# Kernel tuning notes

Hardware: AMD Instinct MI355X
Metric: run time of the kernel (lower is better)

## Reference

```python
import jax, jax.numpy as jnp
import numpy as np

STRIDE = 1  # module init arg


def setup_inputs() -> dict:
    key = jax.random.key(0)
    k1, k2 = jax.random.split(key)
    x = jax.random.normal(k1, (16, 32, 256, 256), dtype=jnp.float32)
    kernel = jax.random.normal(k2, (32, 5, 5), dtype=jnp.float32) * 0.1
    return {"input": x, "kernel": kernel}


def _maxmin_conv(x, kernel, stride=STRIDE):
    # Max-min semifield convolution:
    #   out[b,oc,i,j] = max_{c,dy,dx} min(x_pad[b,c,i*s+dy,j*s+dx], k[oc,dy,dx])
    # Since min(., k) is monotone in x, the max over in-channels commutes:
    #   max_{c} min(x_c, k) == min(max_c x_c, k)
    # so we reduce channels once up front (same math, far less memory).
    K = kernel.shape[-1]
    p = K - 1
    top = p // 2
    bot = p - top  # calculate_padding(): left=top=floor(p/2), right=bottom=p-top
    xmax = jnp.max(x, axis=1)  # [B, H, W]
    xp = jnp.pad(xmax, ((0, 0), (top, bot), (top, bot)), constant_values=-np.inf)
    B, Hp, Wp = xp.shape
    Ho = (Hp - K) // stride + 1
    Wo = (Wp - K) // stride + 1
    OC = kernel.shape[0]
    acc = jnp.full((B, OC, Ho, Wo), -np.inf, dtype=x.dtype)
    for dy in range(K):  # fixed small K*K loop over kernel taps
        for dx in range(K):
            patch = xp[:, dy:dy + stride * Ho:stride, dx:dx + stride * Wo:stride]  # [B,Ho,Wo]
            cand = jnp.minimum(patch[:, None, :, :], kernel[None, :, dy, dx, None, None])
            acc = jnp.maximum(acc, cand)
    return acc


def reference(input, kernel):
    return _maxmin_conv(input, kernel)
```

## Files before the change

### kernel.cpp

```cpp
#include <hip/hip_runtime.h>
#include <math.h>


#define BATCH 16
#define CH    32
#define OCH   32
#define HH    256
#define WW    256
#define HWSZ  (HH * WW)
#define TW    32
#define TH    16
#define LH    20
#define LW    42
#define KP    28
#define NWG   (BATCH * (HH / TH) * (WW / TW))

typedef float floatx4 __attribute__((ext_vector_type(4)));

__device__ __forceinline__ float vmax3(float a, float b, float c) {
    float d;
    asm("v_max3_f32 %0, %1, %2, %3" : "=v"(d) : "v"(a), "v"(b), "v"(c));
    return d;
}

__global__ __launch_bounds__(256, 2) void fused_maxmin_kernel(const float* __restrict__ x,
                                                              const float* __restrict__ kk,
                                                              float* __restrict__ out) {
    __shared__ float xmt[LH][LW];
    __shared__ float lk[OCH * KP];
    int tid = threadIdx.x;
    int bid = blockIdx.x;
    int swz = (bid & 7) * (NWG >> 3) + (bid >> 3);
    int b   = swz >> 7;
    int t2  = swz & 127;
    int ty  = t2 >> 3;
    int tx  = t2 & 7;

    const float NI = -INFINITY;

    for (int i = tid; i < OCH * 25; i += 256)
        lk[(i / 25) * KP + (i % 25)] = kk[i];

    if (tid < 200) {
        int pr = tid / 10;
        int pc = tid % 10;
        int c4 = tx * 8 - 1 + pc;
        int rw = ty * TH - 2 + pr;
        bool valid = (c4 >= 0) && (c4 < WW / 4) && (rw >= 0) && (rw < HH);
        int c4c = c4 < 0 ? 0 : (c4 > WW / 4 - 1 ? WW / 4 - 1 : c4);
        int rwc = rw < 0 ? 0 : (rw > HH - 1 ? HH - 1 : rw);
        const float4* src = (const float4*)x + (size_t)b * CH * (HWSZ / 4)
                          + (size_t)rwc * (WW / 4) + c4c;
        float4 m = src[0];
#pragma unroll
        for (int c = 1; c < CH; ++c) {
            float4 v = src[(size_t)c * (HWSZ / 4)];
            m.x = fmaxf(m.x, v.x);
            m.y = fmaxf(m.y, v.y);
            m.z = fmaxf(m.z, v.z);
            m.w = fmaxf(m.w, v.w);
        }
        if (!valid) { m.x = NI; m.y = NI; m.z = NI; m.w = NI; }
        *(float2*)&xmt[pr][4 * pc]     = make_float2(m.x, m.y);
        *(float2*)&xmt[pr][4 * pc + 2] = make_float2(m.z, m.w);
    }
    __syncthreads();

    int xg = tid & 7;
    int rg = (tid >> 3) & 7;
    int wv = __builtin_amdgcn_readfirstlane(tid >> 6);

    float w[6][8];
#pragma unroll
    for (int r = 0; r < 6; ++r) {
        const float* rp = &xmt[2 * rg + r][4 * xg + 2];
#pragma unroll
        for (int s = 0; s < 4; ++s)
            *(float2*)&w[r][2 * s] = *(const float2*)(rp + 2 * s);
    }

    size_t obase = (size_t)(b * OCH + wv * 8) * HWSZ
                 + (size_t)(ty * TH + 2 * rg) * WW + tx * TW + 4 * xg;

    for (int o = 0; o < 8; ++o) {
        const float* kv = &lk[(wv * 8 + o) * KP];
        float4 q0 = *(const float4*)(kv + 0);
        float4 q1 = *(const float4*)(kv + 4);
        float4 q2 = *(const float4*)(kv + 8);
        float4 q3 = *(const float4*)(kv + 12);
        float4 q4 = *(const float4*)(kv + 16);
        float4 q5 = *(const float4*)(kv + 20);
        float  k24 = kv[24];
        float kr[25] = { q0.x,q0.y,q0.z,q0.w, q1.x,q1.y,q1.z,q1.w,
                         q2.x,q2.y,q2.z,q2.w, q3.x,q3.y,q3.z,q3.w,
                         q4.x,q4.y,q4.z,q4.w, q5.x,q5.y,q5.z,q5.w, k24 };

        float* op = out + obase + (size_t)o * HWSZ;
#pragma unroll
        for (int r = 0; r < 2; ++r) {
            float a[4];
#pragma unroll
            for (int j = 0; j < 4; ++j) {
                float m[25];
#pragma unroll
                for (int dy = 0; dy < 5; ++dy)
#pragma unroll
                    for (int dx = 0; dx < 5; ++dx)
                        m[dy * 5 + dx] = fminf(w[r + dy][j + dx], kr[dy * 5 + dx]);
                float t0 = vmax3(m[0],  m[1],  m[2]);
                float t1 = vmax3(m[3],  m[4],  m[5]);
                float t2 = vmax3(m[6],  m[7],  m[8]);
                float t3 = vmax3(m[9],  m[10], m[11]);
                float t4 = vmax3(m[12], m[13], m[14]);
                float t5 = vmax3(m[15], m[16], m[17]);
                float t6 = vmax3(m[18], m[19], m[20]);
                float t7 = vmax3(m[21], m[22], m[23]);
                float u0 = vmax3(t0, t1, t2);
                float u1 = vmax3(t3, t4, t5);
                float u2 = vmax3(t6, t7, m[24]);
                a[j] = vmax3(u0, u1, u2);
            }
            floatx4 ov = { a[0], a[1], a[2], a[3] };
            __builtin_nontemporal_store(ov, (floatx4*)(op + (size_t)r * WW));
        }
    }
}

extern "C" void kernel_launch(void* const* d_in, const int* in_sizes, int n_in,
                              void* d_out, int out_size, void* d_ws, size_t ws_size,
                              hipStream_t stream) {
    const float* x  = (const float*)d_in[0];
    const float* kk = (const float*)d_in[1];
    float* out      = (float*)d_out;
    fused_maxmin_kernel<<<NWG, 256, 0, stream>>>(x, kk, out);
}
```

Before: 55.27 us.

## Warp-specialize into producer waves and consumer waves with double-buffered LDS tiles

Each workgroup now covers four vertical 16-row tiles and runs 640 threads. Two waves perform the channel-max reduction into a double-buffered shared tile, and eight waves compute the 32 output channels, four each. The intent is to overlap the global-load-heavy reduction with the compute and store phase of the previous tile and to cut the grid to 512 workgroups. The risks are lower occupancy from 640-thread blocks, and the producer waves may become the bottleneck because only 128 threads issue all input loads.

```diff
diff --git a/kernel.cpp b/kernel.cpp
--- a/kernel.cpp
+++ b/kernel.cpp
@@ -8,12 +8,11 @@
 #define HH    256
 #define WW    256
 #define HWSZ  (HH * WW)
-#define TW    32
-#define TH    16
 #define LH    20
 #define LW    42
 #define KP    28
-#define NWG   (BATCH * (HH / TH) * (WW / TW))
+#define NT    4
+#define NWG   512
 
 typedef float floatx4 __attribute__((ext_vector_type(4)));
 
@@ -23,105 +22,150 @@
     return d;
 }
 
-__global__ __launch_bounds__(256, 2) void fused_maxmin_kernel(const float* __restrict__ x,
+__device__ __forceinline__ void lgkm_barrier() {
+    asm volatile("s_waitcnt lgkmcnt(0)" ::: "memory");
+    __builtin_amdgcn_s_barrier();
+}
+
+__global__ __launch_bounds__(640, 5) void fused_maxmin_kernel(const float* __restrict__ x,
                                                               const float* __restrict__ kk,
                                                               float* __restrict__ out) {
-    __shared__ float xmt[LH][LW];
+    __shared__ float xmt[2][LH][LW];
     __shared__ float lk[OCH * KP];
+
     int tid = threadIdx.x;
     int bid = blockIdx.x;
     int swz = (bid & 7) * (NWG >> 3) + (bid >> 3);
-    int b   = swz >> 7;
-    int t2  = swz & 127;
-    int ty  = t2 >> 3;
-    int tx  = t2 & 7;
+    int b   = swz >> 5;
+    int s   = swz & 31;
+    int ys  = s >> 3;
+    int xs  = s & 7;
+    int row0 = ys * 64;
 
     const float NI = -INFINITY;
 
-    for (int i = tid; i < OCH * 25; i += 256)
+    for (int i = tid; i < OCH * 25; i += 640)
         lk[(i / 25) * KP + (i % 25)] = kk[i];
 
-    if (tid < 200) {
-        int pr = tid / 10;
-        int pc = tid % 10;
-        int c4 = tx * 8 - 1 + pc;
-        int rw = ty * TH - 2 + pr;
-        bool valid = (c4 >= 0) && (c4 < WW / 4) && (rw >= 0) && (rw < HH);
-        int c4c = c4 < 0 ? 0 : (c4 > WW / 4 - 1 ? WW / 4 - 1 : c4);
-        int rwc = rw < 0 ? 0 : (rw > HH - 1 ? HH - 1 : rw);
-        const float4* src = (const float4*)x + (size_t)b * CH * (HWSZ / 4)
-                          + (size_t)rwc * (WW / 4) + c4c;
-        float4 m = src[0];
+    const float4* xb4 = (const float4*)x + (size_t)b * CH * (HWSZ / 4);
+    int wave = tid >> 6;
+
+    if (wave < 2) {
+        int pr1 = tid / 10,        pc1 = tid % 10;
+        int g2  = tid + 128;
+        bool has2 = tid < 72;
+        int pr2 = g2 / 10,         pc2 = g2 % 10;
+        int c41 = xs * 8 - 1 + pc1;
+        int c42 = xs * 8 - 1 + pc2;
+        bool cv1 = (c41 >= 0) && (c41 < WW / 4);
+        bool cv2 = (c42 >= 0) && (c42 < WW / 4);
+        int c41c = c41 < 0 ? 0 : (c41 > WW / 4 - 1 ? WW / 4 - 1 : c41);
+        int c42c = c42 < 0 ? 0 : (c42 > WW / 4 - 1 ? WW / 4 - 1 : c42);
+
+        auto produce = [&](int t, int bf) {
+            int ybase = row0 + 16 * t - 2;
+            {
+                int rw = ybase + pr1;
+                bool ok = cv1 && (rw >= 0) && (rw < HH);
+                int rwc = rw < 0 ? 0 : (rw > HH - 1 ? HH - 1 : rw);
+                const float4* src = xb4 + (size_t)rwc * (WW / 4) + c41c;
+                float4 m = src[0];
 #pragma unroll
-        for (int c = 1; c < CH; ++c) {
-            float4 v = src[(size_t)c * (HWSZ / 4)];
-            m.x = fmaxf(m.x, v.x);
-            m.y = fmaxf(m.y, v.y);
-            m.z = fmaxf(m.z, v.z);
-            m.w = fmaxf(m.w, v.w);
+                for (int c = 1; c < CH; ++c) {
+                    float4 v = src[(size_t)c * (HWSZ / 4)];
+                    m.x = fmaxf(m.x, v.x); m.y = fmaxf(m.y, v.y);
+                    m.z = fmaxf(m.z, v.z); m.w = fmaxf(m.w, v.w);
+                }
+                if (!ok) { m.x = NI; m.y = NI; m.z = NI; m.w = NI; }
+                *(float2*)&xmt[bf][pr1][4 * pc1]     = make_float2(m.x, m.y);
+                *(float2*)&xmt[bf][pr1][4 * pc1 + 2] = make_float2(m.z, m.w);
+            }
+            if (has2) {
+                int rw = ybase + pr2;
+                bool ok = cv2 && (rw >= 0) && (rw < HH);
+                int rwc = rw < 0 ? 0 : (rw > HH - 1 ? HH - 1 : rw);
+                const float4* src = xb4 + (size_t)rwc * (WW / 4) + c42c;
+                float4 m = src[0];
+#pragma unroll
+                for (int c = 1; c < CH; ++c) {
+                    float4 v = src[(size_t)c * (HWSZ / 4)];
+                    m.x = fmaxf(m.x, v.x); m.y = fmaxf(m.y, v.y);
+                    m.z = fmaxf(m.z, v.z); m.w = fmaxf(m.w, v.w);
+                }
+                if (!ok) { m.x = NI; m.y = NI; m.z = NI; m.w = NI; }
+                *(float2*)&xmt[bf][pr2][4 * pc2]     = make_float2(m.x, m.y);
+                *(float2*)&xmt[bf][pr2][4 * pc2 + 2] = make_float2(m.z, m.w);
+            }
+        };
+
+        produce(0, 0);
+        lgkm_barrier();
+        for (int t = 0; t < NT; ++t) {
+            if (t + 1 < NT) produce(t + 1, (t + 1) & 1);
+            lgkm_barrier();
         }
-        if (!valid) { m.x = NI; m.y = NI; m.z = NI; m.w = NI; }
-        *(float2*)&xmt[pr][4 * pc]     = make_float2(m.x, m.y);
-        *(float2*)&xmt[pr][4 * pc + 2] = make_float2(m.z, m.w);
-    }
-    __syncthreads();
+    } else {
+        int ctid = tid - 128;
+        int lane = ctid & 63;
+        int cw   = __builtin_amdgcn_readfirstlane(ctid >> 6);
+        int xg   = lane & 7;
+        int rg   = lane >> 3;
+        int ocb  = cw * 4;
 
-    int xg = tid & 7;
-    int rg = (tid >> 3) & 7;
-    int wv = __builtin_amdgcn_readfirstlane(tid >> 6);
-
-    float w[6][8];
+        lgkm_barrier();
+        for (int t = 0; t < NT; ++t) {
+            int bf = t & 1;
+            float w[6][8];
 #pragma unroll
-    for (int r = 0; r < 6; ++r) {
-        const float* rp = &xmt[2 * rg + r][4 * xg + 2];
+            for (int r = 0; r < 6; ++r) {
+                const float* rp = &xmt[bf][2 * rg + r][4 * xg + 2];
 #pragma unroll
-        for (int s = 0; s < 4; ++s)
-            *(float2*)&w[r][2 * s] = *(const float2*)(rp + 2 * s);
-    }
-
-    size_t obase = (size_t)(b * OCH + wv * 8) * HWSZ
-                 + (size_t)(ty * TH + 2 * rg) * WW + tx * TW + 4 * xg;
-
-    for (int o = 0; o < 8; ++o) {
-        const float* kv = &lk[(wv * 8 + o) * KP];
-        float4 q0 = *(const float4*)(kv + 0);
-        float4 q1 = *(const float4*)(kv + 4);
-        float4 q2 = *(const float4*)(kv + 8);
-        float4 q3 = *(const float4*)(kv + 12);
-        float4 q4 = *(const float4*)(kv + 16);
-        float4 q5 = *(const float4*)(kv + 20);
-        float  k24 = kv[24];
-        float kr[25] = { q0.x,q0.y,q0.z,q0.w, q1.x,q1.y,q1.z,q1.w,
-                         q2.x,q2.y,q2.z,q2.w, q3.x,q3.y,q3.z,q3.w,
-                         q4.x,q4.y,q4.z,q4.w, q5.x,q5.y,q5.z,q5.w, k24 };
-
-        float* op = out + obase + (size_t)o * HWSZ;
+                for (int s2 = 0; s2 < 4; ++s2)
+                    *(float2*)&w[r][2 * s2] = *(const float2*)(rp + 2 * s2);
+            }
+            size_t ob = (size_t)(b * OCH + ocb) * HWSZ
+                      + (size_t)(row0 + 16 * t + 2 * rg) * WW + xs * 32 + 4 * xg;
 #pragma unroll
-        for (int r = 0; r < 2; ++r) {
-            float a[4];
+            for (int o = 0; o < 4; ++o) {
+                const float* kv = &lk[(ocb + o) * KP];
+                float4 q0 = *(const float4*)(kv + 0);
+                float4 q1 = *(const float4*)(kv + 4);
+                float4 q2 = *(const float4*)(kv + 8);
+                float4 q3 = *(const float4*)(kv + 12);
+                float4 q4 = *(const float4*)(kv + 16);
+                float4 q5 = *(const float4*)(kv + 20);
+                float  k24 = kv[24];
+                float kr[25] = { q0.x,q0.y,q0.z,q0.w, q1.x,q1.y,q1.z,q1.w,
+                                 q2.x,q2.y,q2.z,q2.w, q3.x,q3.y,q3.z,q3.w,
+                                 q4.x,q4.y,q4.z,q4.w, q5.x,q5.y,q5.z,q5.w, k24 };
+                float* op = out + ob + (size_t)o * HWSZ;
 #pragma unroll
-            for (int j = 0; j < 4; ++j) {
-                float m[25];
+                for (int r = 0; r < 2; ++r) {
+                    float a[4];
 #pragma unroll
-                for (int dy = 0; dy < 5; ++dy)
+                    for (int j = 0; j < 4; ++j) {
+                        float m[25];
 #pragma unroll
-                    for (int dx = 0; dx < 5; ++dx)
-                        m[dy * 5 + dx] = fminf(w[r + dy][j + dx], kr[dy * 5 + dx]);
-                float t0 = vmax3(m[0],  m[1],  m[2]);
-                float t1 = vmax3(m[3],  m[4],  m[5]);
-                float t2 = vmax3(m[6],  m[7],  m[8]);
-                float t3 = vmax3(m[9],  m[10], m[11]);
-                float t4 = vmax3(m[12], m[13], m[14]);
-                float t5 = vmax3(m[15], m[16], m[17]);
-                float t6 = vmax3(m[18], m[19], m[20]);
-                float t7 = vmax3(m[21], m[22], m[23]);
-                float u0 = vmax3(t0, t1, t2);
-                float u1 = vmax3(t3, t4, t5);
-                float u2 = vmax3(t6, t7, m[24]);
-                a[j] = vmax3(u0, u1, u2);
+                        for (int dy = 0; dy < 5; ++dy)
+#pragma unroll
+                            for (int dx = 0; dx < 5; ++dx)
+                                m[dy * 5 + dx] = fminf(w[r + dy][j + dx], kr[dy * 5 + dx]);
+                        float t0 = vmax3(m[0],  m[1],  m[2]);
+                        float t1 = vmax3(m[3],  m[4],  m[5]);
+                        float t2 = vmax3(m[6],  m[7],  m[8]);
+                        float t3 = vmax3(m[9],  m[10], m[11]);
+                        float t4 = vmax3(m[12], m[13], m[14]);
+                        float t5 = vmax3(m[15], m[16], m[17]);
+                        float t6 = vmax3(m[18], m[19], m[20]);
+                        float t7 = vmax3(m[21], m[22], m[23]);
+                        a[j] = vmax3(vmax3(t0, t1, t2), vmax3(t3, t4, t5),
+                                     vmax3(t6, t7, m[24]));
+                    }
+                    floatx4 ov = { a[0], a[1], a[2], a[3] };
+                    __builtin_nontemporal_store(ov, (floatx4*)(op + (size_t)r * WW));
+                }
             }
-            floatx4 ov = { a[0], a[1], a[2], a[3] };
-            __builtin_nontemporal_store(ov, (floatx4*)(op + (size_t)r * WW));
+            lgkm_barrier();
         }
     }
 }
@@ -132,5 +176,5 @@
     const float* x  = (const float*)d_in[0];
     const float* kk = (const float*)d_in[1];
     float* out      = (float*)d_out;
-    fused_maxmin_kernel<<<NWG, 256, 0, stream>>>(x, kk, out);
+    fused_maxmin_kernel<<<NWG, 640, 0, stream>>>(x, kk, out);
 }
```

New measurement: 92.88 us. +68.0%, slower.
